# Optimization experiments

Measured on AMD Instinct MI355X. Metric: run time of the kernel, lower is better.

The kernel has to match this reference:

```python
import jax, jax.numpy as jnp
import numpy as np

N_NODES = 28


def _gcn_norm(edge_index, n):
    """PyG GCNConv normalization: add self-loops, sym-normalize by deg^-1/2."""
    loops = jnp.arange(n, dtype=edge_index.dtype)
    src = jnp.concatenate([edge_index[0], loops])
    dst = jnp.concatenate([edge_index[1], loops])
    ones = jnp.ones(src.shape[0], dtype=jnp.float32)
    deg = jax.ops.segment_sum(ones, dst, num_segments=n)  # in-degree incl. self-loop
    dinv = jnp.where(deg > 0, 1.0 / jnp.sqrt(deg), 0.0)
    norm = dinv[src] * dinv[dst]  # [E+N]
    return src, dst, norm


def _gcn_conv(x, W, b, src, dst, norm, n):
    # x: [B, N, Cin] -> [B, N, Cout]; linear first, then normalized scatter-add.
    h = jnp.einsum('bni,io->bno', x, W)
    msg = h[:, src, :] * norm[None, :, None]          # gather + edge scaling
    out = jnp.zeros_like(h).at[:, dst, :].add(msg)     # scatter-add over dst
    return out + b


def setup_inputs() -> dict:
    key = jax.random.key(0)
    k1, k2, k3, k4 = jax.random.split(key, 4)
    B, N, E, H = 65536, N_NODES, 756, 64
    x = jax.random.normal(k1, (B, N), dtype=jnp.float32)
    edge_index = jax.random.randint(k2, (2, E), 0, N, dtype=jnp.int64)
    W1 = jax.random.normal(k3, (1, H), dtype=jnp.float32) * (1.0 / np.sqrt(1.0))
    b1 = jnp.zeros((H,), dtype=jnp.float32)
    W2 = jax.random.normal(k4, (H, 1), dtype=jnp.float32) * (1.0 / np.sqrt(H))
    b2 = jnp.zeros((1,), dtype=jnp.float32)
    return {"x": x, "edge_index": edge_index, "W1": W1, "b1": b1, "W2": W2, "b2": b2}


def reference(x, edge_index, W1, b1, W2, b2):
    n = x.shape[1]
    src, dst, norm = _gcn_norm(edge_index, n)
    h = x[:, :, None]                                  # [B, N, 1] node features
    h = jax.nn.relu(_gcn_conv(h, W1, b1, src, dst, norm, n))
    # dropout(0.2) is identity in eval mode
    h = _gcn_conv(h, W2, b2, src, dst, norm, n)        # [B, N, 1]
    return h[:, :, 0]
```

## Files before the change

### kernel.cpp

```cpp
#include <hip/hip_runtime.h>
#include <math.h>

#define NN   28
#define NH   64
#define WAVES 8
#define TPB  (WAVES * 64)
#define EPW  16
#define EPB  (WAVES * EPW)
#define ZSTR 29

typedef __attribute__((ext_vector_type(8))) short bf16x8;
typedef __attribute__((ext_vector_type(4))) float f32x4;

static __device__ __forceinline__ short f2bf(float f) {
  unsigned u = __float_as_uint(f);
  u = (u + 0x7FFFu + ((u >> 16) & 1u)) >> 16;
  return (short)u;
}
static __device__ __forceinline__ float bf2f(short h) {
  return __uint_as_float(((unsigned)(unsigned short)h) << 16);
}

__global__ __launch_bounds__(TPB) void gcn_mfma_kernel(
    const float* __restrict__ x, const int* __restrict__ ei, int E,
    const float* __restrict__ W1, const float* __restrict__ b1,
    const float* __restrict__ W2, const float* __restrict__ b2,
    float* __restrict__ out, int B) {
  __shared__ __align__(16) float A[NN * NN];
  __shared__ float dinv[NN];
  __shared__ float cpos_s, cneg_s;
  __shared__ int flag_s;
  __shared__ float zbuf[WAVES][EPW * ZSTR];

  const int t = threadIdx.x;
  const int wave = t >> 6, lane = t & 63;
  const int q = lane >> 4, l15 = lane & 15;

  const int gelem0 = (blockIdx.x * WAVES + wave) * EPW;
  const int me = gelem0 + l15;
  const bool mv = (me < B);
  const float* xr = x + (size_t)(mv ? me : 0) * NN + q * 8;
  float4 xv0 = *(const float4*)xr;
  float4 xv1;
  if (q < 3) xv1 = *(const float4*)(xr + 4);
  else       xv1 = make_float4(0.f, 0.f, 0.f, 0.f);
  if (!mv) { xv0 = make_float4(0.f,0.f,0.f,0.f); xv1 = make_float4(0.f,0.f,0.f,0.f); }

  if (t < NN) dinv[t] = 1.0f;
  for (int i = t; i < NN * NN; i += TPB) A[i] = 0.0f;
  if (t == 0) { cpos_s = 0.0f; cneg_s = 0.0f; flag_s = 0; }
  __syncthreads();

  for (int e = t; e < E; e += TPB) atomicAdd(&dinv[ei[E + e]], 1.0f);
  __syncthreads();
  if (t < NN) dinv[t] = 1.0f / sqrtf(dinv[t]);
  __syncthreads();

  for (int e = t; e < E; e += TPB) {
    int s = ei[e];
    int d = ei[E + e];
    atomicAdd(&A[d * NN + s], dinv[s] * dinv[d]);
  }
  if (t < NN) atomicAdd(&A[t * NN + t], dinv[t] * dinv[t]);

  if (t < NH) {
    float w1 = W1[t], w2 = W2[t];
    if (w1 > 0.0f)      atomicAdd(&cpos_s, w1 * w2);
    else if (w1 < 0.0f) atomicAdd(&cneg_s, w1 * w2);
    if (b1[t] != 0.0f) atomicOr(&flag_s, 1);
  }
  __syncthreads();

  bf16x8 bhi0, bhi1, blo0, blo1;
  {
    const int n0 = l15, n1 = 16 + l15;
#pragma unroll
    for (int j = 0; j < 8; ++j) {
      const int k = q * 8 + j;
      float a0 = (k < NN) ? A[n0 * NN + k] : 0.0f;
      float a1 = (n1 < NN && k < NN) ? A[n1 * NN + k] : 0.0f;
      short h0 = f2bf(a0), h1 = f2bf(a1);
      bhi0[j] = h0; blo0[j] = f2bf(a0 - bf2f(h0));
      bhi1[j] = h1; blo1[j] = f2bf(a1 - bf2f(h1));
    }
  }

  bf16x8 xhi, xlo;
  {
    float xf[8] = {xv0.x, xv0.y, xv0.z, xv0.w, xv1.x, xv1.y, xv1.z, xv1.w};
#pragma unroll
    for (int j = 0; j < 8; ++j) {
      short h = f2bf(xf[j]);
      xhi[j] = h; xlo[j] = f2bf(xf[j] - bf2f(h));
    }
  }

  f32x4 acc0 = {0.f, 0.f, 0.f, 0.f}, acc1 = {0.f, 0.f, 0.f, 0.f};
  acc0 = __builtin_amdgcn_mfma_f32_16x16x32_bf16(xhi, bhi0, acc0, 0, 0, 0);
  acc0 = __builtin_amdgcn_mfma_f32_16x16x32_bf16(xlo, bhi0, acc0, 0, 0, 0);
  acc0 = __builtin_amdgcn_mfma_f32_16x16x32_bf16(xhi, blo0, acc0, 0, 0, 0);
  acc1 = __builtin_amdgcn_mfma_f32_16x16x32_bf16(xhi, bhi1, acc1, 0, 0, 0);
  acc1 = __builtin_amdgcn_mfma_f32_16x16x32_bf16(xlo, bhi1, acc1, 0, 0, 0);
  acc1 = __builtin_amdgcn_mfma_f32_16x16x32_bf16(xhi, blo1, acc1, 0, 0, 0);

  const float cpos = cpos_s, cneg = cneg_s;
  float z0[4], z1[4];
  if (flag_s == 0) {
#pragma unroll
    for (int r = 0; r < 4; ++r) {
      z0[r] = acc0[r] * (acc0[r] > 0.0f ? cpos : cneg);
      z1[r] = acc1[r] * (acc1[r] > 0.0f ? cpos : cneg);
    }
  } else {
#pragma unroll
    for (int r = 0; r < 4; ++r) { z0[r] = 0.0f; z1[r] = 0.0f; }
    for (int o = 0; o < NH; ++o) {
      float w1 = W1[o], bb = b1[o], w2 = W2[o];
#pragma unroll
      for (int r = 0; r < 4; ++r) {
        z0[r] = fmaf(fmaxf(fmaf(acc0[r], w1, bb), 0.0f), w2, z0[r]);
        z1[r] = fmaf(fmaxf(fmaf(acc1[r], w1, bb), 0.0f), w2, z1[r]);
      }
    }
  }

  float* zb = zbuf[wave];
#pragma unroll
  for (int r = 0; r < 4; ++r) {
    const int m = q * 4 + r;
    zb[m * ZSTR + l15] = z0[r];
    if (l15 < NN - 16) zb[m * ZSTR + 16 + l15] = z1[r];
  }
  __builtin_amdgcn_wave_barrier();

  bf16x8 zhi, zlo;
#pragma unroll
  for (int j = 0; j < 8; ++j) {
    const int k = q * 8 + j;
    float v = (k < NN) ? zb[l15 * ZSTR + k] : 0.0f;
    short h = f2bf(v);
    zhi[j] = h; zlo[j] = f2bf(v - bf2f(h));
  }
  __builtin_amdgcn_wave_barrier();

  f32x4 occ0 = {0.f, 0.f, 0.f, 0.f}, occ1 = {0.f, 0.f, 0.f, 0.f};
  occ0 = __builtin_amdgcn_mfma_f32_16x16x32_bf16(zhi, bhi0, occ0, 0, 0, 0);
  occ0 = __builtin_amdgcn_mfma_f32_16x16x32_bf16(zlo, bhi0, occ0, 0, 0, 0);
  occ0 = __builtin_amdgcn_mfma_f32_16x16x32_bf16(zhi, blo0, occ0, 0, 0, 0);
  occ1 = __builtin_amdgcn_mfma_f32_16x16x32_bf16(zhi, bhi1, occ1, 0, 0, 0);
  occ1 = __builtin_amdgcn_mfma_f32_16x16x32_bf16(zlo, bhi1, occ1, 0, 0, 0);
  occ1 = __builtin_amdgcn_mfma_f32_16x16x32_bf16(zhi, blo1, occ1, 0, 0, 0);

  const float bias2 = b2[0];
#pragma unroll
  for (int r = 0; r < 4; ++r) {
    const int m = q * 4 + r;
    zb[m * ZSTR + l15] = occ0[r] + bias2;
    if (l15 < NN - 16) zb[m * ZSTR + 16 + l15] = occ1[r] + bias2;
  }
  __builtin_amdgcn_wave_barrier();

  const size_t obase = (size_t)gelem0 * NN;
  const size_t total = (size_t)B * NN;
#pragma unroll
  for (int k7 = 0; k7 < 7; ++k7) {
    const int flat = lane + 64 * k7;
    const unsigned e = (unsigned)flat / NN;
    const unsigned n = (unsigned)flat - e * NN;
    if (obase + flat < total)
      out[obase + flat] = zb[e * ZSTR + n];
  }
}

extern "C" void kernel_launch(void* const* d_in, const int* in_sizes, int n_in,
                              void* d_out, int out_size, void* d_ws, size_t ws_size,
                              hipStream_t stream) {
  const float* x  = (const float*)d_in[0];
  const int*   ei = (const int*)d_in[1];
  const float* W1 = (const float*)d_in[2];
  const float* b1 = (const float*)d_in[3];
  const float* W2 = (const float*)d_in[4];
  const float* b2 = (const float*)d_in[5];
  float* out = (float*)d_out;

  const int E = in_sizes[1] / 2;
  const int B = in_sizes[0] / NN;

  const int blocks = (B + EPB - 1) / EPB;
  gcn_mfma_kernel<<<blocks, TPB, 0, stream>>>(x, ei, E, W1, b1, W2, b2, out, B);
}
```

Before: 75.27 us.

## Split adjacency/constant build into a one-block prologue kernel read via workspace

The per-block rebuild of the normalized adjacency matrix, the degree atomics and the ReLU-folding constants moves into a single-block setup kernel. That kernel writes pre-split bf16 hi/lo MFMA fragments and scalar constants to workspace. The main kernel loads these fragments directly and no longer does shared-memory atomics or block-wide barriers. Block size also drops from 8 waves to 4. The cost is an extra kernel launch with a serial dependency, plus a global read of the fragments in every wave.

```diff
diff --git a/kernel.cpp b/kernel.cpp
--- a/kernel.cpp
+++ b/kernel.cpp
@@ -3,12 +3,14 @@
 
 #define NN   28
 #define NH   64
-#define WAVES 8
+#define WAVES 4
 #define TPB  (WAVES * 64)
 #define EPW  16
 #define EPB  (WAVES * EPW)
 #define ZSTR 29
 
+#define WS_CONST_OFF 4096
+
 typedef __attribute__((ext_vector_type(8))) short bf16x8;
 typedef __attribute__((ext_vector_type(4))) float f32x4;
 
@@ -21,15 +23,76 @@
   return __uint_as_float(((unsigned)(unsigned short)h) << 16);
 }
 
-__global__ __launch_bounds__(TPB) void gcn_mfma_kernel(
-    const float* __restrict__ x, const int* __restrict__ ei, int E,
+__global__ __launch_bounds__(256) void gcn_build(
+    const int* __restrict__ ei, int E,
     const float* __restrict__ W1, const float* __restrict__ b1,
     const float* __restrict__ W2, const float* __restrict__ b2,
-    float* __restrict__ out, int B) {
+    void* __restrict__ ws) {
   __shared__ __align__(16) float A[NN * NN];
   __shared__ float dinv[NN];
   __shared__ float cpos_s, cneg_s;
   __shared__ int flag_s;
+
+  const int t = threadIdx.x;
+
+  if (t < NN) dinv[t] = 1.0f;
+  for (int i = t; i < NN * NN; i += 256) A[i] = 0.0f;
+  if (t == 0) { cpos_s = 0.0f; cneg_s = 0.0f; flag_s = 0; }
+  __syncthreads();
+
+  for (int e = t; e < E; e += 256) atomicAdd(&dinv[ei[E + e]], 1.0f);
+  __syncthreads();
+  if (t < NN) dinv[t] = 1.0f / sqrtf(dinv[t]);
+  __syncthreads();
+
+  for (int e = t; e < E; e += 256) {
+    int s = ei[e];
+    int d = ei[E + e];
+    atomicAdd(&A[d * NN + s], dinv[s] * dinv[d]);
+  }
+  if (t < NN) atomicAdd(&A[t * NN + t], dinv[t] * dinv[t]);
+
+  if (t < NH) {
+    float w1 = W1[t], w2 = W2[t];
+    if (w1 > 0.0f)      atomicAdd(&cpos_s, w1 * w2);
+    else if (w1 < 0.0f) atomicAdd(&cneg_s, w1 * w2);
+    if (b1[t] != 0.0f) atomicOr(&flag_s, 1);
+  }
+  __syncthreads();
+
+  if (t < 64) {
+    const int q = t >> 4, l15 = t & 15;
+    short frag[32];
+#pragma unroll
+    for (int j = 0; j < 8; ++j) {
+      const int k = q * 8 + j;
+      const int n1 = 16 + l15;
+      float a0 = (k < NN) ? A[l15 * NN + k] : 0.0f;
+      float a1 = (n1 < NN && k < NN) ? A[n1 * NN + k] : 0.0f;
+      short h0 = f2bf(a0), h1 = f2bf(a1);
+      frag[j]      = h0;
+      frag[8 + j]  = f2bf(a0 - bf2f(h0));
+      frag[16 + j] = h1;
+      frag[24 + j] = f2bf(a1 - bf2f(h1));
+    }
+    short* dstp = (short*)ws + t * 32;
+#pragma unroll
+    for (int j = 0; j < 32; ++j) dstp[j] = frag[j];
+  }
+  if (t == 0) {
+    float* c = (float*)((char*)ws + WS_CONST_OFF);
+    c[0] = cpos_s;
+    c[1] = cneg_s;
+    c[2] = b2[0];
+    ((int*)c)[3] = flag_s;
+  }
+}
+
+__global__ __launch_bounds__(TPB) void gcn_main(
+    const float* __restrict__ x, const void* __restrict__ ws,
+    const float* __restrict__ W1, const float* __restrict__ b1,
+    const float* __restrict__ W2,
+    float* __restrict__ out, int B) {
   __shared__ float zbuf[WAVES][EPW * ZSTR];
 
   const int t = threadIdx.x;
@@ -46,44 +109,12 @@
   else       xv1 = make_float4(0.f, 0.f, 0.f, 0.f);
   if (!mv) { xv0 = make_float4(0.f,0.f,0.f,0.f); xv1 = make_float4(0.f,0.f,0.f,0.f); }
 
-  if (t < NN) dinv[t] = 1.0f;
-  for (int i = t; i < NN * NN; i += TPB) A[i] = 0.0f;
-  if (t == 0) { cpos_s = 0.0f; cneg_s = 0.0f; flag_s = 0; }
-  __syncthreads();
-
-  for (int e = t; e < E; e += TPB) atomicAdd(&dinv[ei[E + e]], 1.0f);
-  __syncthreads();
-  if (t < NN) dinv[t] = 1.0f / sqrtf(dinv[t]);
-  __syncthreads();
-
-  for (int e = t; e < E; e += TPB) {
-    int s = ei[e];
-    int d = ei[E + e];
-    atomicAdd(&A[d * NN + s], dinv[s] * dinv[d]);
-  }
-  if (t < NN) atomicAdd(&A[t * NN + t], dinv[t] * dinv[t]);
-
-  if (t < NH) {
-    float w1 = W1[t], w2 = W2[t];
-    if (w1 > 0.0f)      atomicAdd(&cpos_s, w1 * w2);
-    else if (w1 < 0.0f) atomicAdd(&cneg_s, w1 * w2);
-    if (b1[t] != 0.0f) atomicOr(&flag_s, 1);
-  }
-  __syncthreads();
-
-  bf16x8 bhi0, bhi1, blo0, blo1;
-  {
-    const int n0 = l15, n1 = 16 + l15;
-#pragma unroll
-    for (int j = 0; j < 8; ++j) {
-      const int k = q * 8 + j;
-      float a0 = (k < NN) ? A[n0 * NN + k] : 0.0f;
-      float a1 = (n1 < NN && k < NN) ? A[n1 * NN + k] : 0.0f;
-      short h0 = f2bf(a0), h1 = f2bf(a1);
-      bhi0[j] = h0; blo0[j] = f2bf(a0 - bf2f(h0));
-      bhi1[j] = h1; blo1[j] = f2bf(a1 - bf2f(h1));
-    }
-  }
+  const bf16x8* fp = (const bf16x8*)ws + (size_t)lane * 4;
+  const bf16x8 bhi0 = fp[0], blo0 = fp[1], bhi1 = fp[2], blo1 = fp[3];
+
+  const float* cws = (const float*)((const char*)ws + WS_CONST_OFF);
+  const float cpos = cws[0], cneg = cws[1], bias2 = cws[2];
+  const int flag = ((const int*)cws)[3];
 
   bf16x8 xhi, xlo;
   {
@@ -103,9 +134,8 @@
   acc1 = __builtin_amdgcn_mfma_f32_16x16x32_bf16(xlo, bhi1, acc1, 0, 0, 0);
   acc1 = __builtin_amdgcn_mfma_f32_16x16x32_bf16(xhi, blo1, acc1, 0, 0, 0);
 
-  const float cpos = cpos_s, cneg = cneg_s;
   float z0[4], z1[4];
-  if (flag_s == 0) {
+  if (flag == 0) {
 #pragma unroll
     for (int r = 0; r < 4; ++r) {
       z0[r] = acc0[r] * (acc0[r] > 0.0f ? cpos : cneg);
@@ -151,7 +181,6 @@
   occ1 = __builtin_amdgcn_mfma_f32_16x16x32_bf16(zlo, bhi1, occ1, 0, 0, 0);
   occ1 = __builtin_amdgcn_mfma_f32_16x16x32_bf16(zhi, blo1, occ1, 0, 0, 0);
 
-  const float bias2 = b2[0];
 #pragma unroll
   for (int r = 0; r < 4; ++r) {
     const int m = q * 4 + r;
@@ -186,6 +215,8 @@
   const int E = in_sizes[1] / 2;
   const int B = in_sizes[0] / NN;
 
+  gcn_build<<<1, 256, 0, stream>>>(ei, E, W1, b1, W2, b2, d_ws);
+
   const int blocks = (B + EPB - 1) / EPB;
-  gcn_mfma_kernel<<<blocks, TPB, 0, stream>>>(x, ei, E, W1, b1, W2, b2, out, B);
-}
+  gcn_main<<<blocks, TPB, 0, stream>>>(x, d_ws, W1, b1, W2, out, B);
+}
```

Measured after the change: 74.06 us. About the same (-1.6%).
